# Kernel optimization log

Measured on AMD Instinct MI355X. Metric: run time of the kernel, lower is better.

## Reference

```python
import jax, jax.numpy as jnp
import numpy as np

C = 512

def conv1x1(x, w, b):
    # x: [B,C,H,W], w: [O,C], b: [O]
    return jnp.einsum('bchw,oc->bohw', x, w) + b[None, :, None, None]

def setup_inputs() -> dict:
    key = jax.random.key(0)
    ks = jax.random.split(key, 7)
    s = 1.0 / np.sqrt(C)
    x = jax.random.normal(ks[0], (8, C, 64, 64), dtype=jnp.float32)
    wq = jax.random.uniform(ks[1], (C, C), jnp.float32, -s, s)
    bq = jax.random.uniform(ks[2], (C,), jnp.float32, -s, s)
    wk = jax.random.uniform(ks[3], (C, C), jnp.float32, -s, s)
    bk = jax.random.uniform(ks[4], (C,), jnp.float32, -s, s)
    wv = jax.random.uniform(ks[5], (C, C), jnp.float32, -s, s)
    bv = jax.random.uniform(ks[6], (C,), jnp.float32, -s, s)
    return {"x": x, "wq": wq, "bq": bq, "wk": wk, "bk": bk, "wv": wv, "bv": bv}

def reference(x, wq, bq, wk, bk, wv, bv):
    B, Cc, H, W = x.shape
    q = conv1x1(x, wq, bq).reshape(B, Cc, H * W)   # [B,C,N]
    k = conv1x1(x, wk, bk).reshape(B, Cc, H * W)   # [B,C,N]
    v = conv1x1(x, wv, bv).reshape(B, Cc, H * W)   # [B,C,N]
    attn = jnp.einsum('bcn,bdn->bcd', q, k)        # q @ k^T over spatial dim -> [B,C,C]
    attn = jax.nn.softmax(attn, axis=-1)
    out = jnp.einsum('bcd,bdn->bcn', attn, v).reshape(B, Cc, H, W)
    return out + x
```

## Files before the change

### kernel.cpp

```cpp
#include <hip/hip_runtime.h>
#include <cstdint>

typedef unsigned short u16;
typedef unsigned int   u32;
typedef _Float16 f16;

typedef __attribute__((ext_vector_type(8))) _Float16 f16x8;
typedef __attribute__((ext_vector_type(4))) float    f32x4;

__device__ __forceinline__ u16 f2h(float f) {
    union { f16 h; u16 u; } c; c.h = (f16)f; return c.u;
}
__device__ __forceinline__ float h2f(u16 u) {
    union { u16 u; f16 h; } c; c.u = u; return (float)c.h;
}

__device__ __forceinline__ void async_copy16(const u16* g, u16* lds) {
    __builtin_amdgcn_global_load_lds(
        (const __attribute__((address_space(1))) void*)g,
        (__attribute__((address_space(3))) void*)lds,
        16, 0, 0);
}

__device__ __forceinline__ void gemm_nt_f16(
    u16* smem, const u16* __restrict__ A, int lda,
    const u16* __restrict__ B, int ldb, int K, f32x4 acc[4][4])
{
    u16* As = smem; u16* Bs = smem + 4096;
    const int t = threadIdx.x, w = t >> 6, lane = t & 63;
    const int srow = lane >> 2;
    const int skc  = (((lane & 3) ^ ((lane >> 3) & 3)) * 8);
    const int ra0 = (w*2+0)*16 + srow, ra1 = (w*2+1)*16 + srow;
    const u16* gA0 = A + (size_t)ra0 * lda + skc;
    const u16* gA1 = A + (size_t)ra1 * lda + skc;
    const u16* gB0 = B + (size_t)ra0 * ldb + skc;
    const u16* gB1 = B + (size_t)ra1 * ldb + skc;
    u16* lA0 = As + (w*2+0)*512; u16* lA1 = As + (w*2+1)*512;
    u16* lB0 = Bs + (w*2+0)*512; u16* lB1 = Bs + (w*2+1)*512;
    const int fr = lane & 15, fq = lane >> 4;
    const int fc = (fq ^ ((fr >> 1) & 3)) * 8;
    const int wm = (w >> 1) * 64, wn = (w & 1) * 64;
    const u16* fA = As + (wm + fr) * 32 + fc;
    const u16* fB = Bs + (wn + fr) * 32 + fc;

    for (int k0 = 0; k0 < K; k0 += 32) {
        async_copy16(gA0 + k0, lA0);
        async_copy16(gA1 + k0, lA1);
        async_copy16(gB0 + k0, lB0);
        async_copy16(gB1 + k0, lB1);
        __syncthreads();
        f16x8 af[4], bf[4];
#pragma unroll
        for (int i = 0; i < 4; i++) af[i] = *(const f16x8*)(fA + i * 512);
#pragma unroll
        for (int i = 0; i < 4; i++) bf[i] = *(const f16x8*)(fB + i * 512);
#pragma unroll
        for (int mi = 0; mi < 4; mi++)
#pragma unroll
            for (int ni = 0; ni < 4; ni++)
                acc[mi][ni] = __builtin_amdgcn_mfma_f32_16x16x32_f16(
                    af[mi], bf[ni], acc[mi][ni], 0, 0, 0);
        __syncthreads();
    }
}

__device__ __forceinline__ void zero_acc(f32x4 acc[4][4]) {
#pragma unroll
    for (int i = 0; i < 4; i++)
#pragma unroll
        for (int j = 0; j < 4; j++) {
            f32x4 z = {0.f, 0.f, 0.f, 0.f};
            acc[i][j] = z;
        }
}

__global__ __launch_bounds__(256) void k_convw(const float* __restrict__ wq,
                                               const float* __restrict__ wk,
                                               const float* __restrict__ wv,
                                               u16* __restrict__ Wf)
{
    const int t = blockIdx.x * 256 + threadIdx.x;
    const int e = t * 4;
    const int sel = e >> 18;
    const int off = e & 262143;
    const float* src = (sel == 0) ? wq : (sel == 1) ? wk : wv;
    float4 v = *(const float4*)(src + off);
    ushort4 h;
    h.x = f2h(v.x); h.y = f2h(v.y); h.z = f2h(v.z); h.w = f2h(v.w);
    *(ushort4*)(Wf + sel * 262144 + off) = h;
}

__global__ __launch_bounds__(256) void k_transpose(const float* __restrict__ x,
                                                   u16* __restrict__ XT)
{
    __shared__ u16 tile[64][70];
    const int t  = threadIdx.x;
    const int b  = blockIdx.z;
    const int c0 = blockIdx.y * 64;
    const int n0 = blockIdx.x * 64;
    const int rr   = t >> 4;
    const int col4 = (t & 15) * 4;

    const float* src = x + ((size_t)b * 512 + c0) * 4096 + n0;
#pragma unroll
    for (int i = 0; i < 4; i++) {
        int row = i * 16 + rr;
        float4 v = *(const float4*)(src + (size_t)row * 4096 + col4);
        ushort4 h;
        h.x = f2h(v.x); h.y = f2h(v.y); h.z = f2h(v.z); h.w = f2h(v.w);
        *(ushort4*)&tile[row][col4] = h;
    }
    __syncthreads();
    u16* dst = XT + ((size_t)b * 4096 + n0) * 512 + c0;
#pragma unroll
    for (int i = 0; i < 4; i++) {
        int nrow = i * 16 + rr;
        ushort4 o;
        o.x = tile[col4 + 0][nrow];
        o.y = tile[col4 + 1][nrow];
        o.z = tile[col4 + 2][nrow];
        o.w = tile[col4 + 3][nrow];
        *(ushort4*)(dst + (size_t)nrow * 512 + col4) = o;
    }
}

__global__ __launch_bounds__(256) void k_qkv(
    const u16* __restrict__ Wf,
    const float* __restrict__ bq, const float* __restrict__ bk, const float* __restrict__ bv,
    const u16* __restrict__ XT,
    u16* __restrict__ Qh, u16* __restrict__ Kh, u16* __restrict__ VT)
{
    __shared__ u16 smem[8192];
    const int n0  = blockIdx.x * 128;
    const int my  = blockIdx.y;
    const int b   = blockIdx.z;
    const int sel = my >> 2;
    const int m0  = (my & 3) * 128;

    const float* bi = (sel == 0) ? bq : (sel == 1) ? bk : bv;
    const u16* Ap = Wf + (size_t)sel * 262144 + (size_t)m0 * 512;
    const u16* Bp = XT + ((size_t)b * 4096 + n0) * 512;

    f32x4 acc[4][4];
    zero_acc(acc);
    gemm_nt_f16(smem, Ap, 512, Bp, 512, 512, acc);

    const int t = threadIdx.x, w = t >> 6, lane = t & 63;
    const int wm = (w >> 1) * 64, wn = (w & 1) * 64;
    const int cn = lane & 15, cq = lane >> 4;

    if (sel < 2) {
        u16* out = ((sel == 0) ? Qh : Kh) + (size_t)b * 512 * 4096;
#pragma unroll
        for (int mi = 0; mi < 4; mi++)
#pragma unroll
            for (int ni = 0; ni < 4; ni++)
#pragma unroll
                for (int r = 0; r < 4; r++) {
                    int m = wm + mi * 16 + cq * 4 + r;
                    int n = wn + ni * 16 + cn;
                    out[(size_t)(m0 + m) * 4096 + n0 + n] =
                        f2h(acc[mi][ni][r] + bi[m0 + m]);
                }
    } else {
        u16* out = VT + (size_t)b * 4096 * 512;
#pragma unroll
        for (int mi = 0; mi < 4; mi++)
#pragma unroll
            for (int ni = 0; ni < 4; ni++) {
                int n  = wn + ni * 16 + cn;
                int mb = wm + mi * 16 + cq * 4;
                ushort4 pk;
                pk.x = f2h(acc[mi][ni][0] + bi[m0 + mb + 0]);
                pk.y = f2h(acc[mi][ni][1] + bi[m0 + mb + 1]);
                pk.z = f2h(acc[mi][ni][2] + bi[m0 + mb + 2]);
                pk.w = f2h(acc[mi][ni][3] + bi[m0 + mb + 3]);
                *(ushort4*)(out + (size_t)(n0 + n) * 512 + m0 + mb) = pk;
            }
    }
}

__global__ __launch_bounds__(256) void k_scores(const u16* __restrict__ Qh,
                                                const u16* __restrict__ Kh,
                                                float* __restrict__ S)
{
    __shared__ u16 smem[8192];
    const int n0 = blockIdx.x * 128;
    const int m0 = blockIdx.y * 128;
    const int bz = blockIdx.z;
    const int b  = bz >> 2, ks = bz & 3;

    const u16* Ap = Qh + (size_t)b * 512 * 4096 + (size_t)m0 * 4096 + ks * 1024;
    const u16* Bp = Kh + (size_t)b * 512 * 4096 + (size_t)n0 * 4096 + ks * 1024;

    f32x4 acc[4][4];
    zero_acc(acc);
    gemm_nt_f16(smem, Ap, 4096, Bp, 4096, 1024, acc);

    const int t = threadIdx.x, w = t >> 6, lane = t & 63;
    const int wm = (w >> 1) * 64, wn = (w & 1) * 64;
    const int cn = lane & 15, cq = lane >> 4;

    float* out = S + ((size_t)(ks * 8 + b) * 512 + m0) * 512 + n0;
#pragma unroll
    for (int mi = 0; mi < 4; mi++)
#pragma unroll
        for (int ni = 0; ni < 4; ni++)
#pragma unroll
            for (int r = 0; r < 4; r++) {
                int m = wm + mi * 16 + cq * 4 + r;
                int n = wn + ni * 16 + cn;
                out[(size_t)m * 512 + n] = acc[mi][ni][r];
            }
}

__global__ __launch_bounds__(256) void k_softmax(const float* __restrict__ S,
                                                 u16* __restrict__ P)
{
    const int row = blockIdx.x;
    const int t = threadIdx.x, w = t >> 6, lane = t & 63;
    const size_t st = (size_t)8 * 512 * 512;
    const float* r0 = S + (size_t)row * 512;

    float v0 = r0[t]       + r0[t + st]       + r0[t + 2*st]       + r0[t + 3*st];
    float v1 = r0[t + 256] + r0[t + 256 + st] + r0[t + 256 + 2*st] + r0[t + 256 + 3*st];

    float m = fmaxf(v0, v1);
    for (int o = 32; o; o >>= 1) m = fmaxf(m, __shfl_xor(m, o));
    __shared__ float redm[4];
    if (lane == 0) redm[w] = m;
    __syncthreads();
    m = fmaxf(fmaxf(redm[0], redm[1]), fmaxf(redm[2], redm[3]));

    float e0 = __expf(v0 - m), e1 = __expf(v1 - m);
    float s = e0 + e1;
    for (int o = 32; o; o >>= 1) s += __shfl_xor(s, o);
    __shared__ float reds[4];
    if (lane == 0) reds[w] = s;
    __syncthreads();
    s = reds[0] + reds[1] + reds[2] + reds[3];

    float inv = 1.0f / s;
    P[(size_t)row * 512 + t]       = f2h(e0 * inv);
    P[(size_t)row * 512 + t + 256] = f2h(e1 * inv);
}

__global__ __launch_bounds__(256) void k_out(const u16* __restrict__ P,
                                             const u16* __restrict__ VT,
                                             const float* __restrict__ x,
                                             float* __restrict__ out)
{
    __shared__ u16 smem[8192];
    const int n0 = blockIdx.x * 128;
    const int m0 = blockIdx.y * 128;
    const int b  = blockIdx.z;

    const u16* Ap = P  + (size_t)b * 512 * 512 + (size_t)m0 * 512;
    const u16* Bp = VT + (size_t)b * 4096 * 512 + (size_t)n0 * 512;

    f32x4 acc[4][4];
    zero_acc(acc);
    gemm_nt_f16(smem, Ap, 512, Bp, 512, 512, acc);

    const int t = threadIdx.x, w = t >> 6, lane = t & 63;
    const int wm = (w >> 1) * 64, wn = (w & 1) * 64;
    const int cn = lane & 15, cq = lane >> 4;

#pragma unroll
    for (int mi = 0; mi < 4; mi++)
#pragma unroll
        for (int ni = 0; ni < 4; ni++)
#pragma unroll
            for (int r = 0; r < 4; r++) {
                int m = wm + mi * 16 + cq * 4 + r;
                int n = wn + ni * 16 + cn;
                size_t idx = ((size_t)b * 512 + m0 + m) * 4096 + n0 + n;
                out[idx] = acc[mi][ni][r] + x[idx];
            }
}

extern "C" void kernel_launch(void* const* d_in, const int* in_sizes, int n_in,
                              void* d_out, int out_size, void* d_ws, size_t ws_size,
                              hipStream_t stream)
{
    const float* x  = (const float*)d_in[0];
    const float* wq = (const float*)d_in[1];
    const float* bq = (const float*)d_in[2];
    const float* wk = (const float*)d_in[3];
    const float* bk = (const float*)d_in[4];
    const float* wv = (const float*)d_in[5];
    const float* bv = (const float*)d_in[6];
    float* out = (float*)d_out;

    char* ws = (char*)d_ws;
    u16*  Wf = (u16*)(ws);
    u16*  XT = (u16*)(ws + 1572864);
    u16*  Qh = (u16*)(ws + 35127296);
    u16*  Kh = (u16*)(ws + 68681728);
    u16*  VT = (u16*)(ws + 102236160);
    float* S = (float*)(ws + 1572864);
    u16*  P  = (u16*)(ws + 135790592);

    k_convw<<<dim3(768), dim3(256), 0, stream>>>(wq, wk, wv, Wf);
    k_transpose<<<dim3(64, 8, 8), dim3(256), 0, stream>>>(x, XT);
    k_qkv<<<dim3(32, 12, 8), dim3(256), 0, stream>>>(Wf, bq, bk, bv, XT, Qh, Kh, VT);
    k_scores<<<dim3(4, 4, 32), dim3(256), 0, stream>>>(Qh, Kh, S);
    k_softmax<<<dim3(4096), dim3(256), 0, stream>>>(S, P);
    k_out<<<dim3(32, 4, 8), dim3(256), 0, stream>>>(P, VT, x, out);
}
```

Baseline: 292.1 us.

## Reformulate channel attention via Gram matrix of x to skip Q/K/V projections

Result: faster. 267.3 us (-8.5%).

```diff
diff --git a/kernel.cpp b/kernel.cpp
--- a/kernel.cpp
+++ b/kernel.cpp
@@ -76,22 +76,61 @@
 
 __global__ __launch_bounds__(256) void k_convw(const float* __restrict__ wq,
                                                const float* __restrict__ wk,
-                                               const float* __restrict__ wv,
-                                               u16* __restrict__ Wf)
+                                               u16* __restrict__ Wq2,
+                                               u16* __restrict__ Wkh,
+                                               float* __restrict__ s)
 {
     const int t = blockIdx.x * 256 + threadIdx.x;
+    if (t < 4096) s[t] = 0.f;
     const int e = t * 4;
     const int sel = e >> 18;
     const int off = e & 262143;
-    const float* src = (sel == 0) ? wq : (sel == 1) ? wk : wv;
+    const float* src = sel ? wk : wq;
     float4 v = *(const float4*)(src + off);
     ushort4 h;
     h.x = f2h(v.x); h.y = f2h(v.y); h.z = f2h(v.z); h.w = f2h(v.w);
-    *(ushort4*)(Wf + sel * 262144 + off) = h;
-}
-
-__global__ __launch_bounds__(256) void k_transpose(const float* __restrict__ x,
-                                                   u16* __restrict__ XT)
+    if (sel == 0) {
+        int i = off >> 9, c = off & 511;
+        *(ushort4*)(Wq2 + (size_t)i * 1024 + c) = h;
+        *(ushort4*)(Wq2 + (size_t)i * 1024 + 512 + c) = h;
+    } else {
+        *(ushort4*)(Wkh + off) = h;
+    }
+}
+
+__global__ __launch_bounds__(256) void k_wvt(const float* __restrict__ wv,
+                                             u16* __restrict__ WvT)
+{
+    __shared__ u16 tile[64][70];
+    const int t = threadIdx.x;
+    const int d0 = blockIdx.y * 64;
+    const int c0 = blockIdx.x * 64;
+    const int rr = t >> 4, col4 = (t & 15) * 4;
+#pragma unroll
+    for (int i = 0; i < 4; i++) {
+        int row = i * 16 + rr;
+        float4 v = *(const float4*)(wv + (size_t)(d0 + row) * 512 + c0 + col4);
+        ushort4 h;
+        h.x = f2h(v.x); h.y = f2h(v.y); h.z = f2h(v.z); h.w = f2h(v.w);
+        *(ushort4*)&tile[row][col4] = h;
+    }
+    __syncthreads();
+#pragma unroll
+    for (int i = 0; i < 4; i++) {
+        int crow = i * 16 + rr;
+        ushort4 o;
+        o.x = tile[col4 + 0][crow];
+        o.y = tile[col4 + 1][crow];
+        o.z = tile[col4 + 2][crow];
+        o.w = tile[col4 + 3][crow];
+        *(ushort4*)(WvT + (size_t)(c0 + crow) * 512 + d0 + col4) = o;
+    }
+}
+
+__global__ __launch_bounds__(256) void k_convx(const float* __restrict__ x,
+                                               u16* __restrict__ Xh,
+                                               u16* __restrict__ XT,
+                                               float* __restrict__ s)
 {
     __shared__ u16 tile[64][70];
     const int t  = threadIdx.x;
@@ -102,6 +141,7 @@
     const int col4 = (t & 15) * 4;
 
     const float* src = x + ((size_t)b * 512 + c0) * 4096 + n0;
+    u16* xh = Xh + ((size_t)b * 512 + c0) * 4096 + n0;
 #pragma unroll
     for (int i = 0; i < 4; i++) {
         int row = i * 16 + rr;
@@ -109,6 +149,11 @@
         ushort4 h;
         h.x = f2h(v.x); h.y = f2h(v.y); h.z = f2h(v.z); h.w = f2h(v.w);
         *(ushort4*)&tile[row][col4] = h;
+        *(ushort4*)(xh + (size_t)row * 4096 + col4) = h;
+        float p = v.x + v.y + v.z + v.w;
+        p += __shfl_xor(p, 1); p += __shfl_xor(p, 2);
+        p += __shfl_xor(p, 4); p += __shfl_xor(p, 8);
+        if ((t & 15) == 0) atomicAdd(&s[b * 512 + c0 + row], p);
     }
     __syncthreads();
     u16* dst = XT + ((size_t)b * 4096 + n0) * 512 + c0;
@@ -124,65 +169,8 @@
     }
 }
 
-__global__ __launch_bounds__(256) void k_qkv(
-    const u16* __restrict__ Wf,
-    const float* __restrict__ bq, const float* __restrict__ bk, const float* __restrict__ bv,
-    const u16* __restrict__ XT,
-    u16* __restrict__ Qh, u16* __restrict__ Kh, u16* __restrict__ VT)
-{
-    __shared__ u16 smem[8192];
-    const int n0  = blockIdx.x * 128;
-    const int my  = blockIdx.y;
-    const int b   = blockIdx.z;
-    const int sel = my >> 2;
-    const int m0  = (my & 3) * 128;
-
-    const float* bi = (sel == 0) ? bq : (sel == 1) ? bk : bv;
-    const u16* Ap = Wf + (size_t)sel * 262144 + (size_t)m0 * 512;
-    const u16* Bp = XT + ((size_t)b * 4096 + n0) * 512;
-
-    f32x4 acc[4][4];
-    zero_acc(acc);
-    gemm_nt_f16(smem, Ap, 512, Bp, 512, 512, acc);
-
-    const int t = threadIdx.x, w = t >> 6, lane = t & 63;
-    const int wm = (w >> 1) * 64, wn = (w & 1) * 64;
-    const int cn = lane & 15, cq = lane >> 4;
-
-    if (sel < 2) {
-        u16* out = ((sel == 0) ? Qh : Kh) + (size_t)b * 512 * 4096;
-#pragma unroll
-        for (int mi = 0; mi < 4; mi++)
-#pragma unroll
-            for (int ni = 0; ni < 4; ni++)
-#pragma unroll
-                for (int r = 0; r < 4; r++) {
-                    int m = wm + mi * 16 + cq * 4 + r;
-                    int n = wn + ni * 16 + cn;
-                    out[(size_t)(m0 + m) * 4096 + n0 + n] =
-                        f2h(acc[mi][ni][r] + bi[m0 + m]);
-                }
-    } else {
-        u16* out = VT + (size_t)b * 4096 * 512;
-#pragma unroll
-        for (int mi = 0; mi < 4; mi++)
-#pragma unroll
-            for (int ni = 0; ni < 4; ni++) {
-                int n  = wn + ni * 16 + cn;
-                int mb = wm + mi * 16 + cq * 4;
-                ushort4 pk;
-                pk.x = f2h(acc[mi][ni][0] + bi[m0 + mb + 0]);
-                pk.y = f2h(acc[mi][ni][1] + bi[m0 + mb + 1]);
-                pk.z = f2h(acc[mi][ni][2] + bi[m0 + mb + 2]);
-                pk.w = f2h(acc[mi][ni][3] + bi[m0 + mb + 3]);
-                *(ushort4*)(out + (size_t)(n0 + n) * 512 + m0 + mb) = pk;
-            }
-    }
-}
-
-__global__ __launch_bounds__(256) void k_scores(const u16* __restrict__ Qh,
-                                                const u16* __restrict__ Kh,
-                                                float* __restrict__ S)
+__global__ __launch_bounds__(256) void k_gram(const u16* __restrict__ Xh,
+                                              float* __restrict__ Gp)
 {
     __shared__ u16 smem[8192];
     const int n0 = blockIdx.x * 128;
@@ -190,8 +178,8 @@
     const int bz = blockIdx.z;
     const int b  = bz >> 2, ks = bz & 3;
 
-    const u16* Ap = Qh + (size_t)b * 512 * 4096 + (size_t)m0 * 4096 + ks * 1024;
-    const u16* Bp = Kh + (size_t)b * 512 * 4096 + (size_t)n0 * 4096 + ks * 1024;
+    const u16* Ap = Xh + (size_t)b * 512 * 4096 + (size_t)m0 * 4096 + ks * 1024;
+    const u16* Bp = Xh + (size_t)b * 512 * 4096 + (size_t)n0 * 4096 + ks * 1024;
 
     f32x4 acc[4][4];
     zero_acc(acc);
@@ -201,7 +189,7 @@
     const int wm = (w >> 1) * 64, wn = (w & 1) * 64;
     const int cn = lane & 15, cq = lane >> 4;
 
-    float* out = S + ((size_t)(ks * 8 + b) * 512 + m0) * 512 + n0;
+    float* outp = Gp + ((size_t)(ks * 8 + b) * 512 + m0) * 512 + n0;
 #pragma unroll
     for (int mi = 0; mi < 4; mi++)
 #pragma unroll
@@ -210,53 +198,231 @@
             for (int r = 0; r < 4; r++) {
                 int m = wm + mi * 16 + cq * 4 + r;
                 int n = wn + ni * 16 + cn;
-                out[(size_t)m * 512 + n] = acc[mi][ni][r];
+                outp[(size_t)m * 512 + n] = acc[mi][ni][r];
             }
 }
 
-__global__ __launch_bounds__(256) void k_softmax(const float* __restrict__ S,
-                                                 u16* __restrict__ P)
-{
-    const int row = blockIdx.x;
-    const int t = threadIdx.x, w = t >> 6, lane = t & 63;
+__global__ __launch_bounds__(256) void k_gred(const float* __restrict__ Gp,
+                                              u16* __restrict__ Ghl)
+{
+    const size_t idx = ((size_t)blockIdx.x * 256 + threadIdx.x) * 4;
     const size_t st = (size_t)8 * 512 * 512;
-    const float* r0 = S + (size_t)row * 512;
-
-    float v0 = r0[t]       + r0[t + st]       + r0[t + 2*st]       + r0[t + 3*st];
-    float v1 = r0[t + 256] + r0[t + 256 + st] + r0[t + 256 + 2*st] + r0[t + 256 + 3*st];
-
-    float m = fmaxf(v0, v1);
-    for (int o = 32; o; o >>= 1) m = fmaxf(m, __shfl_xor(m, o));
-    __shared__ float redm[4];
-    if (lane == 0) redm[w] = m;
-    __syncthreads();
-    m = fmaxf(fmaxf(redm[0], redm[1]), fmaxf(redm[2], redm[3]));
-
-    float e0 = __expf(v0 - m), e1 = __expf(v1 - m);
-    float s = e0 + e1;
-    for (int o = 32; o; o >>= 1) s += __shfl_xor(s, o);
-    __shared__ float reds[4];
-    if (lane == 0) reds[w] = s;
-    __syncthreads();
-    s = reds[0] + reds[1] + reds[2] + reds[3];
-
-    float inv = 1.0f / s;
-    P[(size_t)row * 512 + t]       = f2h(e0 * inv);
-    P[(size_t)row * 512 + t + 256] = f2h(e1 * inv);
-}
-
-__global__ __launch_bounds__(256) void k_out(const u16* __restrict__ P,
-                                             const u16* __restrict__ VT,
-                                             const float* __restrict__ x,
-                                             float* __restrict__ out)
+    float4 g0 = *(const float4*)(Gp + idx);
+    float4 g1 = *(const float4*)(Gp + idx + st);
+    float4 g2 = *(const float4*)(Gp + idx + 2 * st);
+    float4 g3 = *(const float4*)(Gp + idx + 3 * st);
+    float gx = g0.x + g1.x + g2.x + g3.x;
+    float gy = g0.y + g1.y + g2.y + g3.y;
+    float gz = g0.z + g1.z + g2.z + g3.z;
+    float gw = g0.w + g1.w + g2.w + g3.w;
+    ushort4 hi, lo;
+    hi.x = f2h(gx); lo.x = f2h(gx - h2f(hi.x));
+    hi.y = f2h(gy); lo.y = f2h(gy - h2f(hi.y));
+    hi.z = f2h(gz); lo.z = f2h(gz - h2f(hi.z));
+    hi.w = f2h(gw); lo.w = f2h(gw - h2f(hi.w));
+    const size_t row = idx >> 9;
+    const int c = (int)(idx & 511);
+    *(ushort4*)(Ghl + row * 1024 + c) = hi;
+    *(ushort4*)(Ghl + row * 1024 + 512 + c) = lo;
+}
+
+__global__ __launch_bounds__(256) void k_uv(const float* __restrict__ wq,
+                                            const float* __restrict__ bq,
+                                            const float* __restrict__ wk,
+                                            const float* __restrict__ s,
+                                            float* __restrict__ ubar,
+                                            float* __restrict__ vv)
+{
+    const int b = blockIdx.y;
+    const int which = blockIdx.x >> 3;
+    const int r0 = (blockIdx.x & 7) * 64;
+    const int t = threadIdx.x;
+    const int i = r0 + (t >> 2), l4 = t & 3;
+    const float* W = which ? wk : wq;
+    const float* sb = s + b * 512;
+    float acc = 0.f;
+#pragma unroll 4
+    for (int k = 0; k < 32; k++) {
+        int c = k * 16 + l4 * 4;
+        float4 w4 = *(const float4*)(W + (size_t)i * 512 + c);
+        float4 s4 = *(const float4*)(sb + c);
+        acc += w4.x * s4.x + w4.y * s4.y + w4.z * s4.z + w4.w * s4.w;
+    }
+    acc += __shfl_xor(acc, 1);
+    acc += __shfl_xor(acc, 2);
+    if (l4 == 0) {
+        if (which) vv[b * 512 + i] = acc;
+        else       ubar[b * 512 + i] = acc + 4096.0f * bq[i];
+    }
+}
+
+__global__ __launch_bounds__(256) void k_T(const u16* __restrict__ Wq2,
+                                           const u16* __restrict__ Ghl,
+                                           u16* __restrict__ Tb)
 {
     __shared__ u16 smem[8192];
     const int n0 = blockIdx.x * 128;
     const int m0 = blockIdx.y * 128;
     const int b  = blockIdx.z;
 
-    const u16* Ap = P  + (size_t)b * 512 * 512 + (size_t)m0 * 512;
-    const u16* Bp = VT + (size_t)b * 4096 * 512 + (size_t)n0 * 512;
+    const u16* Ap = Wq2 + (size_t)m0 * 1024;
+    const u16* Bp = Ghl + (size_t)b * 512 * 1024 + (size_t)n0 * 1024;
+
+    f32x4 acc[4][4];
+    zero_acc(acc);
+    gemm_nt_f16(smem, Ap, 1024, Bp, 1024, 1024, acc);
+
+    const int t = threadIdx.x, w = t >> 6, lane = t & 63;
+    const int wm = (w >> 1) * 64, wn = (w & 1) * 64;
+    const int cn = lane & 15, cq = lane >> 4;
+
+    u16* outp = Tb + ((size_t)b * 512 + m0) * 512 + n0;
+#pragma unroll
+    for (int mi = 0; mi < 4; mi++)
+#pragma unroll
+        for (int ni = 0; ni < 4; ni++)
+#pragma unroll
+            for (int r = 0; r < 4; r++) {
+                int m = wm + mi * 16 + cq * 4 + r;
+                int n = wn + ni * 16 + cn;
+                outp[(size_t)m * 512 + n] = f2h(acc[mi][ni][r]);
+            }
+}
+
+__global__ __launch_bounds__(256) void k_S(
+    const u16* __restrict__ Tb, const u16* __restrict__ Wkh,
+    const float* __restrict__ ubar, const float* __restrict__ vv,
+    const float* __restrict__ bq, const float* __restrict__ bk,
+    const float* __restrict__ bv,
+    u16* __restrict__ P, float* __restrict__ pbv)
+{
+    __shared__ u16 smem[16896];
+    __shared__ float redm[16][4];
+    __shared__ float reds[16][4][2];
+    u16* As = smem; u16* Bs = smem + 512;
+
+    const int m0 = blockIdx.x * 16;
+    const int b  = blockIdx.y;
+    const int t = threadIdx.x, w = t >> 6, lane = t & 63;
+    const int srow = lane >> 2;
+    const int schunk = ((lane & 3) ^ ((srow >> 1) & 3)) * 8;
+    const u16* gA = Tb + ((size_t)b * 512 + m0 + srow) * 512 + schunk;
+    const int fr = lane & 15, fq = lane >> 4;
+    const int fc = (fq ^ ((fr >> 1) & 3)) * 8;
+
+    f32x4 acc[8];
+#pragma unroll
+    for (int i = 0; i < 8; i++) { f32x4 z = {0.f,0.f,0.f,0.f}; acc[i] = z; }
+
+    for (int k0 = 0; k0 < 512; k0 += 32) {
+        if (w == 0) async_copy16(gA + k0, As);
+#pragma unroll
+        for (int ii = 0; ii < 8; ii++) {
+            int rbase = w * 128 + ii * 16;
+            async_copy16(Wkh + (size_t)(rbase + srow) * 512 + k0 + schunk,
+                         Bs + rbase * 32);
+        }
+        __syncthreads();
+        f16x8 af = *(const f16x8*)(As + fr * 32 + fc);
+#pragma unroll
+        for (int ni = 0; ni < 8; ni++) {
+            f16x8 bf = *(const f16x8*)(Bs + (w * 128 + ni * 16 + fr) * 32 + fc);
+            acc[ni] = __builtin_amdgcn_mfma_f32_16x16x32_f16(af, bf, acc[ni], 0, 0, 0);
+        }
+        __syncthreads();
+    }
+
+    const int cn = lane & 15, cq = lane >> 4;
+    float ub[4], bqr[4];
+#pragma unroll
+    for (int r = 0; r < 4; r++) {
+        int i = m0 + cq * 4 + r;
+        ub[r]  = ubar[b * 512 + i];
+        bqr[r] = bq[i];
+    }
+    float vj[8], bkj[8], bvj[8];
+#pragma unroll
+    for (int ni = 0; ni < 8; ni++) {
+        int j = w * 128 + ni * 16 + cn;
+        vj[ni]  = vv[b * 512 + j];
+        bkj[ni] = bk[j];
+        bvj[ni] = bv[j];
+    }
+    float sv[8][4], mr[4];
+#pragma unroll
+    for (int r = 0; r < 4; r++) mr[r] = -1e30f;
+#pragma unroll
+    for (int ni = 0; ni < 8; ni++)
+#pragma unroll
+        for (int r = 0; r < 4; r++) {
+            sv[ni][r] = acc[ni][r] + ub[r] * bkj[ni] + bqr[r] * vj[ni];
+            mr[r] = fmaxf(mr[r], sv[ni][r]);
+        }
+#pragma unroll
+    for (int r = 0; r < 4; r++)
+        for (int o = 1; o < 16; o <<= 1) mr[r] = fmaxf(mr[r], __shfl_xor(mr[r], o));
+    if (cn == 0) {
+#pragma unroll
+        for (int r = 0; r < 4; r++) redm[cq * 4 + r][w] = mr[r];
+    }
+    __syncthreads();
+#pragma unroll
+    for (int r = 0; r < 4; r++) {
+        int row = cq * 4 + r;
+        mr[r] = fmaxf(fmaxf(redm[row][0], redm[row][1]),
+                      fmaxf(redm[row][2], redm[row][3]));
+    }
+    float e[8][4], se[4], sebv[4];
+#pragma unroll
+    for (int r = 0; r < 4; r++) { se[r] = 0.f; sebv[r] = 0.f; }
+#pragma unroll
+    for (int ni = 0; ni < 8; ni++)
+#pragma unroll
+        for (int r = 0; r < 4; r++) {
+            float ev = __expf(sv[ni][r] - mr[r]);
+            e[ni][r] = ev;
+            se[r]   += ev;
+            sebv[r] += ev * bvj[ni];
+        }
+#pragma unroll
+    for (int r = 0; r < 4; r++)
+        for (int o = 1; o < 16; o <<= 1) {
+            se[r]   += __shfl_xor(se[r], o);
+            sebv[r] += __shfl_xor(sebv[r], o);
+        }
+    if (cn == 0) {
+#pragma unroll
+        for (int r = 0; r < 4; r++) {
+            reds[cq * 4 + r][w][0] = se[r];
+            reds[cq * 4 + r][w][1] = sebv[r];
+        }
+    }
+    __syncthreads();
+#pragma unroll
+    for (int r = 0; r < 4; r++) {
+        int row = cq * 4 + r;
+        float S  = reds[row][0][0] + reds[row][1][0] + reds[row][2][0] + reds[row][3][0];
+        float SB = reds[row][0][1] + reds[row][1][1] + reds[row][2][1] + reds[row][3][1];
+        float inv = 1.0f / S;
+#pragma unroll
+        for (int ni = 0; ni < 8; ni++)
+            P[((size_t)b * 512 + m0 + row) * 512 + w * 128 + ni * 16 + cn] =
+                f2h(e[ni][r] * inv);
+        if (w == 0 && cn == 0) pbv[b * 512 + m0 + row] = SB * inv;
+    }
+}
+
+__global__ __launch_bounds__(256) void k_M(const u16* __restrict__ P,
+                                           const u16* __restrict__ WvT,
+                                           u16* __restrict__ M2)
+{
+    __shared__ u16 smem[8192];
+    const int n0 = blockIdx.x * 128;
+    const int m0 = blockIdx.y * 128;
+    const int b  = blockIdx.z;
+
+    const u16* Ap = P + (size_t)b * 512 * 512 + (size_t)m0 * 512;
+    const u16* Bp = WvT + (size_t)n0 * 512;
 
     f32x4 acc[4][4];
     zero_acc(acc);
@@ -266,6 +432,7 @@
     const int wm = (w >> 1) * 64, wn = (w & 1) * 64;
     const int cn = lane & 15, cq = lane >> 4;
 
+    u16* outp = M2 + ((size_t)b * 512 + m0) * 512 + n0;
 #pragma unroll
     for (int mi = 0; mi < 4; mi++)
 #pragma unroll
@@ -274,8 +441,42 @@
             for (int r = 0; r < 4; r++) {
                 int m = wm + mi * 16 + cq * 4 + r;
                 int n = wn + ni * 16 + cn;
-                size_t idx = ((size_t)b * 512 + m0 + m) * 4096 + n0 + n;
-                out[idx] = acc[mi][ni][r] + x[idx];
+                outp[(size_t)m * 512 + n] = f2h(acc[mi][ni][r]);
+            }
+}
+
+__global__ __launch_bounds__(256) void k_out(const u16* __restrict__ M2,
+                                             const u16* __restrict__ XT,
+                                             const u16* __restrict__ Xh,
+                                             const float* __restrict__ pbv,
+                                             float* __restrict__ out)
+{
+    __shared__ u16 smem[8192];
+    const int n0 = blockIdx.x * 128;
+    const int m0 = blockIdx.y * 128;
+    const int b  = blockIdx.z;
+
+    const u16* Ap = M2 + (size_t)b * 512 * 512 + (size_t)m0 * 512;
+    const u16* Bp = XT + (size_t)b * 4096 * 512 + (size_t)n0 * 512;
+
+    f32x4 acc[4][4];
+    zero_acc(acc);
+    gemm_nt_f16(smem, Ap, 512, Bp, 512, 512, acc);
+
+    const int t = threadIdx.x, w = t >> 6, lane = t & 63;
+    const int wm = (w >> 1) * 64, wn = (w & 1) * 64;
+    const int cn = lane & 15, cq = lane >> 4;
+
+#pragma unroll
+    for (int mi = 0; mi < 4; mi++)
+#pragma unroll
+        for (int ni = 0; ni < 4; ni++)
+#pragma unroll
+            for (int r = 0; r < 4; r++) {
+                int m = m0 + wm + mi * 16 + cq * 4 + r;
+                int n = n0 + wn + ni * 16 + cn;
+                size_t idx = ((size_t)b * 512 + m) * 4096 + n;
+                out[idx] = acc[mi][ni][r] + pbv[b * 512 + m] + h2f(Xh[idx]);
             }
 }
 
@@ -293,18 +494,29 @@
     float* out = (float*)d_out;
 
     char* ws = (char*)d_ws;
-    u16*  Wf = (u16*)(ws);
-    u16*  XT = (u16*)(ws + 1572864);
-    u16*  Qh = (u16*)(ws + 35127296);
-    u16*  Kh = (u16*)(ws + 68681728);
-    u16*  VT = (u16*)(ws + 102236160);
-    float* S = (float*)(ws + 1572864);
-    u16*  P  = (u16*)(ws + 135790592);
-
-    k_convw<<<dim3(768), dim3(256), 0, stream>>>(wq, wk, wv, Wf);
-    k_transpose<<<dim3(64, 8, 8), dim3(256), 0, stream>>>(x, XT);
-    k_qkv<<<dim3(32, 12, 8), dim3(256), 0, stream>>>(Wf, bq, bk, bv, XT, Qh, Kh, VT);
-    k_scores<<<dim3(4, 4, 32), dim3(256), 0, stream>>>(Qh, Kh, S);
-    k_softmax<<<dim3(4096), dim3(256), 0, stream>>>(S, P);
-    k_out<<<dim3(32, 4, 8), dim3(256), 0, stream>>>(P, VT, x, out);
-}
+    u16*   Wq2  = (u16*)(ws);
+    u16*   Wkh  = (u16*)(ws + 1048576);
+    u16*   WvT  = (u16*)(ws + 1572864);
+    float* s    = (float*)(ws + 2097152);
+    float* ubar = (float*)(ws + 2113536);
+    float* vv   = (float*)(ws + 2129920);
+    float* pbv  = (float*)(ws + 2146304);
+    u16*   Xh   = (u16*)(ws + 2162688);
+    u16*   XT   = (u16*)(ws + 35717120);
+    float* Gp   = (float*)(ws + 69271552);
+    u16*   Ghl  = (u16*)(ws + 102825984);
+    u16*   Tb   = (u16*)(ws + 111214592);
+    u16*   P    = (u16*)(ws + 115408896);
+    u16*   M2   = (u16*)(ws + 119603200);
+
+    k_convw<<<dim3(512), dim3(256), 0, stream>>>(wq, wk, Wq2, Wkh, s);
+    k_wvt<<<dim3(8, 8), dim3(256), 0, stream>>>(wv, WvT);
+    k_convx<<<dim3(64, 8, 8), dim3(256), 0, stream>>>(x, Xh, XT, s);
+    k_gram<<<dim3(4, 4, 32), dim3(256), 0, stream>>>(Xh, Gp);
+    k_gred<<<dim3(2048), dim3(256), 0, stream>>>(Gp, Ghl);
+    k_uv<<<dim3(16, 8), dim3(256), 0, stream>>>(wq, bq, wk, s, ubar, vv);
+    k_T<<<dim3(4, 4, 8), dim3(256), 0, stream>>>(Wq2, Ghl, Tb);
+    k_S<<<dim3(32, 8), dim3(256), 0, stream>>>(Tb, Wkh, ubar, vv, bq, bk, bv, P, pbv);
+    k_M<<<dim3(4, 4, 8), dim3(256), 0, stream>>>(P, WvT, M2);
+    k_out<<<dim3(32, 4, 8), dim3(256), 0, stream>>>(M2, XT, Xh, pbv, out);
+}
```
